# Kernel tuning notes

Hardware: AMD Instinct MI355X
Metric: run time of the kernel (lower is better)

The kernel has to match this reference:

```python
import jax, jax.numpy as jnp
import numpy as np
import math

EMBED_DIM = 768
HIDDEN_DIM = 96
N_HEAD = 8
BATCH = 32
K_LEN = 512
Q_LEN = 512


def setup_inputs() -> dict:
    key = jax.random.key(0)
    k1, k2, k3, k4 = jax.random.split(key, 4)
    k = jax.random.normal(k1, (BATCH, K_LEN, EMBED_DIM), dtype=jnp.float32)
    q = jax.random.normal(k2, (BATCH, Q_LEN, EMBED_DIM), dtype=jnp.float32)
    # per-head projection weights, as in nn.Parameter(torch.FloatTensor(n_head, embed_dim, hidden_dim))
    w_kx = jax.random.normal(k3, (N_HEAD, EMBED_DIM, HIDDEN_DIM), dtype=jnp.float32) * (1.0 / math.sqrt(EMBED_DIM))
    w_qx = jax.random.normal(k4, (N_HEAD, EMBED_DIM, HIDDEN_DIM), dtype=jnp.float32) * (1.0 / math.sqrt(EMBED_DIM))
    return {"k": k, "q": q, "w_kx": w_kx, "w_qx": w_qx}


def reference(k, q, w_kx, w_qx):
    # scaled_dot_product variant of ABSA-PyTorch Attention.
    mb, k_len, _ = k.shape
    q_len = q.shape[1]
    hidden = w_kx.shape[-1]
    # per-head projections: [h, b, len, d]  (torch: repeat over heads + bmm)
    kx = jnp.einsum('bke,hed->hbkd', k, w_kx)
    qx = jnp.einsum('bqe,hed->hbqd', q, w_qx)
    # scores [h, b, q, k], scaled
    score = jnp.einsum('hbqd,hbkd->hbqk', qx, kx) / jnp.sqrt(jnp.asarray(hidden, kx.dtype))
    attn = jax.nn.softmax(score, axis=-1)
    # weighted sum over the PROJECTED keys (kx), as in the original: bmm(score, kx)
    out = jnp.einsum('hbqk,hbkd->hbqd', attn, kx)
    # torch.cat(torch.split(output, mb, dim=0), dim=-1): concat heads on last dim
    out = jnp.transpose(out, (1, 2, 0, 3)).reshape(mb, q_len, w_kx.shape[0] * hidden)
    return out
```

## Files before the change

### kernel.cpp

```cpp
#include <hip/hip_runtime.h>
#include <hip/hip_bf16.h>

typedef short short8 __attribute__((ext_vector_type(8)));
typedef short short4v __attribute__((ext_vector_type(4)));
typedef float floatx4 __attribute__((ext_vector_type(4)));

#define EMB 768
#define DH 96
#define NHEAD 8
#define NBATCH 32
#define SEQ 512
#define MROWS (NBATCH * SEQ)

__device__ __forceinline__ unsigned short f2bf(float x) {
    __hip_bfloat16 h = __float2bfloat16(x);
    union { __hip_bfloat16 b; unsigned short u; } c;
    c.b = h;
    return c.u;
}

__global__ __launch_bounds__(256) void cvt_w_kernel(
    const float* __restrict__ wk, const float* __restrict__ wq,
    unsigned short* __restrict__ wtk, unsigned short* __restrict__ wtq)
{
    __shared__ float ws[64][97];
    const int h = blockIdx.x, et = blockIdx.y;
    const float* wsrc = (blockIdx.z ? wq : wk) + (size_t)h * EMB * DH;
    unsigned short* o = blockIdx.z ? wtq : wtk;
    const int t = threadIdx.x;
    const int e0 = et * 64;
    #pragma unroll
    for (int i = 0; i < 6; ++i) {
        int f = i * 256 + t;
        int e = f / 24, c = f % 24;
        float4 v = *(const float4*)(wsrc + (size_t)(e0 + e) * DH + c * 4);
        ws[e][c*4+0] = v.x; ws[e][c*4+1] = v.y; ws[e][c*4+2] = v.z; ws[e][c*4+3] = v.w;
    }
    __syncthreads();
    #pragma unroll
    for (int i = 0; i < 3; ++i) {
        int f = i * 256 + t;
        int d = f >> 3, c8 = f & 7;
        short8 v;
        #pragma unroll
        for (int j = 0; j < 8; ++j) v[j] = (short)f2bf(ws[c8*8+j][d]);
        *(short8*)(o + (size_t)(h*DH + d) * EMB + e0 + c8*8) = v;
    }
}

__global__ __launch_bounds__(256, 2) void proj_kernel(
    const float* __restrict__ x,
    const unsigned short* __restrict__ wt,
    unsigned short* __restrict__ xp)
{
    __shared__ char As[16384];
    __shared__ char Bs[32768];
    const int t = threadIdx.x;
    const int wv = t >> 6, l = t & 63;
    const int lr = l & 15, lg = l >> 4, l7 = l & 7;
    const int mt = blockIdx.x * 128, nt = blockIdx.y * 256;
    const int mw = (wv >> 1) * 64, nw = (wv & 1) * 128;

    floatx4 acc[4][8];
    #pragma unroll
    for (int a = 0; a < 4; ++a)
        #pragma unroll
        for (int b = 0; b < 8; ++b) acc[a][b] = (floatx4){0.f, 0.f, 0.f, 0.f};

    for (int kt = 0; kt < EMB / 64; ++kt) {
        __syncthreads();
        #pragma unroll
        for (int i = 0; i < 4; ++i) {
            int f = i * 256 + t;
            int row = f >> 3, s = f & 7;
            const float* xs = x + (size_t)(mt + row) * EMB + kt*64 + s*8;
            float4 ga = *(const float4*)xs;
            float4 gb = *(const float4*)(xs + 4);
            union { unsigned short h[8]; short8 s8; } pk;
            pk.h[0] = f2bf(ga.x); pk.h[1] = f2bf(ga.y);
            pk.h[2] = f2bf(ga.z); pk.h[3] = f2bf(ga.w);
            pk.h[4] = f2bf(gb.x); pk.h[5] = f2bf(gb.y);
            pk.h[6] = f2bf(gb.z); pk.h[7] = f2bf(gb.w);
            *(short8*)(As + row*128 + ((s ^ (row & 7)) * 16)) = pk.s8;
        }
        #pragma unroll
        for (int i = 0; i < 8; ++i) {
            int f = i * 256 + t;
            int row = f >> 3, s = f & 7;
            short8 gw = *(const short8*)(wt + (size_t)(nt + row) * EMB + kt*64 + s*8);
            *(short8*)(Bs + row*128 + ((s ^ (row & 7)) * 16)) = gw;
        }
        __syncthreads();
        #pragma unroll
        for (int ks = 0; ks < 2; ++ks) {
            const int sl = (ks*4 + lg) ^ l7;
            short8 af[4], bf[8];
            #pragma unroll
            for (int mf = 0; mf < 4; ++mf)
                af[mf] = *(const short8*)(As + (mw + 16*mf + lr) * 128 + sl*16);
            #pragma unroll
            for (int nf = 0; nf < 8; ++nf)
                bf[nf] = *(const short8*)(Bs + (nw + 16*nf + lr) * 128 + sl*16);
            #pragma unroll
            for (int mf = 0; mf < 4; ++mf)
                #pragma unroll
                for (int nf = 0; nf < 8; ++nf)
                    acc[mf][nf] = __builtin_amdgcn_mfma_f32_16x16x32_bf16(
                        af[mf], bf[nf], acc[mf][nf], 0, 0, 0);
        }
    }
    #pragma unroll
    for (int mf = 0; mf < 4; ++mf)
        #pragma unroll
        for (int r = 0; r < 4; ++r) {
            int m = mt + mw + 16*mf + lg*4 + r;
            unsigned short* op = xp + (size_t)m * EMB + nt + nw + lr;
            #pragma unroll
            for (int nf = 0; nf < 8; ++nf) op[16*nf] = f2bf(acc[mf][nf][r]);
        }
}

__global__ __launch_bounds__(256) void attn_kernel(
    const unsigned short* __restrict__ kx,
    const unsigned short* __restrict__ qx,
    float* __restrict__ out)
{
    __shared__ char Ks[64 * 192];
    __shared__ char Kt2[16 * 768];
    const int t = threadIdx.x;
    const int wv = t >> 6, l = t & 63;
    const int lr = l & 15, lg = l >> 4;
    const int q0 = blockIdx.x * 256, b = blockIdx.y, h = blockIdx.z;
    const size_t bq = (size_t)b * SEQ;
    const int hcol = h * DH;
    const float scale = 0.10206207261596575f;

    short8 qf[4][3];
    #pragma unroll
    for (int mf = 0; mf < 4; ++mf)
        #pragma unroll
        for (int ks = 0; ks < 3; ++ks)
            qf[mf][ks] = *(const short8*)(qx
                + (bq + q0 + 64*wv + 16*mf + lr) * EMB + hcol + ks*32 + lg*8);

    floatx4 of[4][6];
    #pragma unroll
    for (int mf = 0; mf < 4; ++mf)
        #pragma unroll
        for (int dt = 0; dt < 6; ++dt) of[mf][dt] = (floatx4){0.f, 0.f, 0.f, 0.f};
    float lsum[4] = {0.f, 0.f, 0.f, 0.f};

    for (int kt = 0; kt < SEQ / 64; ++kt) {
        __syncthreads();
        #pragma unroll
        for (int i = 0; i < 2; ++i) {
            int f = i * 256 + t;
            if (f < 384) {
                int rp = f / 12, s = f - rp * 12;
                int r0 = rp * 2;
                const unsigned short* src = kx + (bq + kt*64 + r0) * EMB + hcol + s*8;
                short8 g0 = *(const short8*)src;
                short8 g1 = *(const short8*)(src + EMB);
                *(short8*)(Ks + r0*192 + ((s + r0) % 12) * 16) = g0;
                *(short8*)(Ks + (r0+1)*192 + ((s + r0 + 1) % 12) * 16) = g1;
                const int c = rp >> 1, tau = 5 * (c & 3);
                char* kb = Kt2 + c*768 + ((rp & 1) << 2);
                #pragma unroll
                for (int j = 0; j < 8; ++j) {
                    int d = s*8 + j;
                    unsigned int pr = (unsigned int)(unsigned short)g0[j]
                                    | ((unsigned int)(unsigned short)g1[j] << 16);
                    *(unsigned int*)(kb + ((d ^ tau) << 3)) = pr;
                }
            }
        }
        __syncthreads();

        floatx4 sf[4][4];
        #pragma unroll
        for (int mf = 0; mf < 4; ++mf)
            #pragma unroll
            for (int nf = 0; nf < 4; ++nf) sf[mf][nf] = (floatx4){0.f, 0.f, 0.f, 0.f};
        __builtin_amdgcn_s_setprio(1);
        #pragma unroll
        for (int ks = 0; ks < 3; ++ks) {
            short8 bk[4];
            #pragma unroll
            for (int nf = 0; nf < 4; ++nf) {
                int row = 16*nf + lr;
                bk[nf] = *(const short8*)(Ks + row*192 + ((ks*4 + lg + row) % 12) * 16);
            }
            #pragma unroll
            for (int mf = 0; mf < 4; ++mf)
                #pragma unroll
                for (int nf = 0; nf < 4; ++nf)
                    sf[mf][nf] = __builtin_amdgcn_mfma_f32_16x16x32_bf16(
                        bk[nf], qf[mf][ks], sf[mf][nf], 0, 0, 0);
        }
        __builtin_amdgcn_s_setprio(0);

        #pragma unroll
        for (int mf = 0; mf < 4; ++mf)
            #pragma unroll
            for (int nf = 0; nf < 4; ++nf)
                #pragma unroll
                for (int r = 0; r < 4; ++r) {
                    float p = __expf(fmaf(sf[mf][nf][r], scale, -12.0f));
                    sf[mf][nf][r] = p;
                    lsum[mf] += p;
                }

        #pragma unroll
        for (int ks2 = 0; ks2 < 2; ++ks2) {
            union { unsigned short hsh[8]; short8 s8; } ap[4];
            #pragma unroll
            for (int mf = 0; mf < 4; ++mf)
                #pragma unroll
                for (int j = 0; j < 8; ++j)
                    ap[mf].hsh[j] = f2bf(sf[mf][2*ks2 + (j >> 2)][j & 3]);
            const int cbase = (8*ks2 + lg) * 768;
            const int tau = 5 * lg;
            __builtin_amdgcn_s_setprio(1);
            #pragma unroll
            for (int dt = 0; dt < 6; ++dt) {
                const int gofs = ((16*dt + lr) ^ tau) << 3;
                short4v lo = *(const short4v*)(Kt2 + cbase + gofs);
                short4v hi = *(const short4v*)(Kt2 + cbase + 3072 + gofs);
                short8 bv;
                bv[0] = lo[0]; bv[1] = lo[1]; bv[2] = lo[2]; bv[3] = lo[3];
                bv[4] = hi[0]; bv[5] = hi[1]; bv[6] = hi[2]; bv[7] = hi[3];
                #pragma unroll
                for (int mf = 0; mf < 4; ++mf)
                    of[mf][dt] = __builtin_amdgcn_mfma_f32_16x16x32_bf16(
                        ap[mf].s8, bv, of[mf][dt], 0, 0, 0);
            }
            __builtin_amdgcn_s_setprio(0);
        }
    }

    float invq[4];
    #pragma unroll
    for (int mf = 0; mf < 4; ++mf) {
        float v = lsum[mf];
        v += __shfl_xor(v, 16);
        v += __shfl_xor(v, 32);
        invq[mf] = 1.0f / v;
    }
    #pragma unroll
    for (int mf = 0; mf < 4; ++mf)
        #pragma unroll
        for (int r = 0; r < 4; ++r) {
            float inv = __shfl(invq[mf], 4*lg + r);
            int q = q0 + 64*wv + 16*mf + 4*lg + r;
            float* op = out + (bq + q) * (NHEAD*DH) + hcol + lr;
            #pragma unroll
            for (int dt = 0; dt < 6; ++dt) op[16*dt] = of[mf][dt][r] * inv;
        }
}

extern "C" void kernel_launch(void* const* d_in, const int* in_sizes, int n_in,
                              void* d_out, int out_size, void* d_ws, size_t ws_size,
                              hipStream_t stream) {
    const float* kin = (const float*)d_in[0];
    const float* qin = (const float*)d_in[1];
    const float* wk  = (const float*)d_in[2];
    const float* wq  = (const float*)d_in[3];
    float* out = (float*)d_out;

    unsigned short* wsu = (unsigned short*)d_ws;
    const size_t SZX = (size_t)MROWS * EMB;
    unsigned short* kxb = wsu;
    unsigned short* qxb = wsu + SZX;
    unsigned short* wtk = wsu + 2*SZX;
    unsigned short* wtq = wtk + (size_t)EMB * (NHEAD*DH);

    cvt_w_kernel<<<dim3(NHEAD, EMB/64, 2), 256, 0, stream>>>(wk, wq, wtk, wtq);
    proj_kernel<<<dim3(MROWS/128, (NHEAD*DH)/256), 256, 0, stream>>>(kin, wtk, kxb);
    proj_kernel<<<dim3(MROWS/128, (NHEAD*DH)/256), 256, 0, stream>>>(qin, wtq, qxb);
    attn_kernel<<<dim3(SEQ/256, NBATCH, NHEAD), 256, 0, stream>>>(kxb, qxb, out);
}
```

Baseline: 128.0 us.

## Prefetch next K-tile into registers in projection GEMM; drop setprio hints

The projection GEMM now loads the next 64-wide K-slice of activations and weights into registers while the current slice is computed, instead of loading right before storing to shared memory. This lets global memory latency overlap the MFMA work of the previous iteration. The cost is many more live registers (32 floats plus 32 shorts per thread on top of a 128-float accumulator), which may lower occupancy or cause spills. The attention kernel also loses its s_setprio wave-priority hints around its MFMA loops.

```diff
diff --git a/kernel.cpp b/kernel.cpp
--- a/kernel.cpp
+++ b/kernel.cpp
@@ -67,15 +67,30 @@
         #pragma unroll
         for (int b = 0; b < 8; ++b) acc[a][b] = (floatx4){0.f, 0.f, 0.f, 0.f};
 
+    float4 pA[4][2];
+    short8 pB[8];
+    #pragma unroll
+    for (int i = 0; i < 4; ++i) {
+        int f = i * 256 + t;
+        int row = f >> 3, s = f & 7;
+        const float* xs = x + (size_t)(mt + row) * EMB + s*8;
+        pA[i][0] = *(const float4*)xs;
+        pA[i][1] = *(const float4*)(xs + 4);
+    }
+    #pragma unroll
+    for (int i = 0; i < 8; ++i) {
+        int f = i * 256 + t;
+        int row = f >> 3, s = f & 7;
+        pB[i] = *(const short8*)(wt + (size_t)(nt + row) * EMB + s*8);
+    }
+
     for (int kt = 0; kt < EMB / 64; ++kt) {
         __syncthreads();
         #pragma unroll
         for (int i = 0; i < 4; ++i) {
             int f = i * 256 + t;
             int row = f >> 3, s = f & 7;
-            const float* xs = x + (size_t)(mt + row) * EMB + kt*64 + s*8;
-            float4 ga = *(const float4*)xs;
-            float4 gb = *(const float4*)(xs + 4);
+            float4 ga = pA[i][0], gb = pA[i][1];
             union { unsigned short h[8]; short8 s8; } pk;
             pk.h[0] = f2bf(ga.x); pk.h[1] = f2bf(ga.y);
             pk.h[2] = f2bf(ga.z); pk.h[3] = f2bf(ga.w);
@@ -87,8 +102,24 @@
         for (int i = 0; i < 8; ++i) {
             int f = i * 256 + t;
             int row = f >> 3, s = f & 7;
-            short8 gw = *(const short8*)(wt + (size_t)(nt + row) * EMB + kt*64 + s*8);
-            *(short8*)(Bs + row*128 + ((s ^ (row & 7)) * 16)) = gw;
+            *(short8*)(Bs + row*128 + ((s ^ (row & 7)) * 16)) = pB[i];
+        }
+        if (kt < EMB/64 - 1) {
+            const int ktn = kt + 1;
+            #pragma unroll
+            for (int i = 0; i < 4; ++i) {
+                int f = i * 256 + t;
+                int row = f >> 3, s = f & 7;
+                const float* xs = x + (size_t)(mt + row) * EMB + ktn*64 + s*8;
+                pA[i][0] = *(const float4*)xs;
+                pA[i][1] = *(const float4*)(xs + 4);
+            }
+            #pragma unroll
+            for (int i = 0; i < 8; ++i) {
+                int f = i * 256 + t;
+                int row = f >> 3, s = f & 7;
+                pB[i] = *(const short8*)(wt + (size_t)(nt + row) * EMB + ktn*64 + s*8);
+            }
         }
         __syncthreads();
         #pragma unroll
@@ -181,7 +212,6 @@
         for (int mf = 0; mf < 4; ++mf)
             #pragma unroll
             for (int nf = 0; nf < 4; ++nf) sf[mf][nf] = (floatx4){0.f, 0.f, 0.f, 0.f};
-        __builtin_amdgcn_s_setprio(1);
         #pragma unroll
         for (int ks = 0; ks < 3; ++ks) {
             short8 bk[4];
@@ -197,7 +227,6 @@
                     sf[mf][nf] = __builtin_amdgcn_mfma_f32_16x16x32_bf16(
                         bk[nf], qf[mf][ks], sf[mf][nf], 0, 0, 0);
         }
-        __builtin_amdgcn_s_setprio(0);
 
         #pragma unroll
         for (int mf = 0; mf < 4; ++mf)
@@ -220,7 +249,6 @@
                     ap[mf].hsh[j] = f2bf(sf[mf][2*ks2 + (j >> 2)][j & 3]);
             const int cbase = (8*ks2 + lg) * 768;
             const int tau = 5 * lg;
-            __builtin_amdgcn_s_setprio(1);
             #pragma unroll
             for (int dt = 0; dt < 6; ++dt) {
                 const int gofs = ((16*dt + lr) ^ tau) << 3;
@@ -234,7 +262,6 @@
                     of[mf][dt] = __builtin_amdgcn_mfma_f32_16x16x32_bf16(
                         ap[mf].s8, bv, of[mf][dt], 0, 0, 0);
             }
-            __builtin_amdgcn_s_setprio(0);
         }
     }
 
```

Result: slower. 150.2 us (+17.4%).
